# Performance work log

Hardware: AMD Instinct MI355X
Metric: run time of the kernel (lower is better)

Reference implementation:

```python
import jax, jax.numpy as jnp
import numpy as np
from itertools import product

L0 = (41, 1600, 1408)  # sparse_shape (z,y,x) from pc_range / voxel_size + [1,0,0]
B = 4
N_PER = 25000
PNAMES = ['w_in','s_in','b_in','w1','s1','b1','w2a','s2a','b2a','w2b','s2b','b2b','w2c','s2c','b2c','w3a','s3a','b3a','w3b','s3b','b3b','w3c','s3c','b3c','w4a','s4a','b4a','w4b','s4b','b4b','w4c','s4c','b4c','w_out','s_out','b_out']


def _enc(c, shape):
    D, H, W = shape
    return ((c[:, 0].astype(np.int64) * D + c[:, 1]) * H + c[:, 2]) * W + c[:, 3]


def _subm_rb(coords, shape):
    # submanifold conv rulebook: out site i gathers input j with coord_j = coord_i + offset
    N = coords.shape[0]
    keys = _enc(coords, shape)
    order = np.argsort(keys); sk = keys[order]
    ins, outs = [], []
    for dz, dy, dx in product((-1, 0, 1), repeat=3):
        nb = coords.astype(np.int64).copy()
        nb[:, 1] += dz; nb[:, 2] += dy; nb[:, 3] += dx
        ok = ((nb[:, 1] >= 0) & (nb[:, 1] < shape[0]) & (nb[:, 2] >= 0) & (nb[:, 2] < shape[1]) & (nb[:, 3] >= 0) & (nb[:, 3] < shape[2]))
        qi = np.nonzero(ok)[0]
        qk = _enc(nb[qi], shape)
        pos = np.clip(np.searchsorted(sk, qk), 0, N - 1)
        f = sk[pos] == qk
        ins.append(order[pos[f]].astype(np.int32))
        outs.append(qi[f].astype(np.int32))
    R = max(len(a) for a in ins)
    rin = np.zeros((27, R), np.int32); rout = np.full((27, R), N, np.int32)  # pad -> dummy out row
    for k in range(27):
        rin[k, :len(ins[k])] = ins[k]; rout[k, :len(outs[k])] = outs[k]
    return jnp.asarray(rin), jnp.asarray(rout)


def _spconv_rb(coords, shape, ks, st, pd):
    # strided sparse conv: out = (in + pad - k) / stride where divisible and in-bounds
    osh = tuple((shape[i] + 2 * pd[i] - ks[i]) // st[i] + 1 for i in range(3))
    per = []; allk = []
    for off in product(*[range(k) for k in ks]):
        oc = np.empty((coords.shape[0], 4), np.int64)
        oc[:, 0] = coords[:, 0]
        ok = np.ones(coords.shape[0], bool)
        for d in range(3):
            v = coords[:, d + 1].astype(np.int64) + pd[d] - off[d]
            ok &= (v % st[d] == 0)
            v = v // st[d]
            ok &= (v >= 0) & (v < osh[d])
            oc[:, d + 1] = v
        qi = np.nonzero(ok)[0]
        qk = _enc(oc[qi], osh)
        per.append((qi.astype(np.int32), qk)); allk.append(qk)
    uk = np.unique(np.concatenate(allk))
    Nout = len(uk); K = len(per)
    R = max(len(qi) for qi, _ in per)
    rin = np.zeros((K, R), np.int32); rout = np.full((K, R), Nout, np.int32)
    for k, (qi, qk) in enumerate(per):
        rin[k, :len(qi)] = qi
        rout[k, :len(qi)] = np.searchsorted(uk, qk).astype(np.int32)
    t = uk.copy()
    x = t % osh[2]; t //= osh[2]; y = t % osh[1]; t //= osh[1]; z = t % osh[0]; b = t // osh[0]
    ocoords = np.stack([b, z, y, x], 1).astype(np.int32)
    return jnp.asarray(rin), jnp.asarray(rout), ocoords, osh


def _gen_coords(rng):
    # clustered LiDAR-like voxel occupancy: gaussian clusters so 3x3x3 neighborhoods are populated
    out = []
    for b in range(B):
        nc = 250
        ctr = np.stack([rng.integers(6, 34, nc), rng.integers(60, 1540, nc), rng.integers(60, 1348, nc)], 1)
        pts = ctr[np.repeat(np.arange(nc), 400)] + rng.normal(0.0, 2.0, (nc * 400, 3))
        pts = np.rint(pts).astype(np.int64)
        for d in range(3):
            pts[:, d] = np.clip(pts[:, d], 0, L0[d] - 1)
        keys = (pts[:, 0] * L0[1] + pts[:, 1]) * L0[2] + pts[:, 2]
        _, ui = np.unique(keys, return_index=True)
        assert len(ui) >= N_PER
        c = pts[np.sort(ui[:N_PER])]
        out.append(np.concatenate([np.full((N_PER, 1), b, np.int64), c], 1))
    return np.concatenate(out, 0).astype(np.int32)


def _conv(feat, W, rin, rout, nout):
    # gather -> per-offset GEMM -> scatter-add (spconv rulebook algorithm)
    out = jnp.zeros((nout + 1, W.shape[2]), feat.dtype)  # +1 dummy row for padding
    for k in range(W.shape[0]):
        out = out.at[rout[k]].add(feat[rin[k]] @ W[k])
    return out[:nout]


def _bnrelu(x, s, b):
    # eval-mode BatchNorm1d folded to affine, then ReLU
    return jax.nn.relu(x * s + b)


def _net(voxels, normalizer, rb1_in, rb1_out, rb2s_in, rb2s_out, batch2, rb2_in, rb2_out, rb3s_in, rb3s_out, batch3, rb3_in, rb3_out, rb4s_in, rb4s_out, batch4, rb4_in, rb4_out, rbo_in, rbo_out, batch_out, P):
    n0 = voxels.shape[0]; n2 = batch2.shape[0]; n3 = batch3.shape[0]; n4 = batch4.shape[0]; no = batch_out.shape[0]
    f = voxels.sum(1) / normalizer  # mean VFE: (N0, 4)
    x = _bnrelu(_conv(f, P['w_in'], rb1_in, rb1_out, n0), P['s_in'], P['b_in'])
    x = _bnrelu(_conv(x, P['w1'], rb1_in, rb1_out, n0), P['s1'], P['b1'])
    x = _bnrelu(_conv(x, P['w2a'], rb2s_in, rb2s_out, n2), P['s2a'], P['b2a'])
    x = _bnrelu(_conv(x, P['w2b'], rb2_in, rb2_out, n2), P['s2b'], P['b2b'])
    x = _bnrelu(_conv(x, P['w2c'], rb2_in, rb2_out, n2), P['s2c'], P['b2c'])
    x = _bnrelu(_conv(x, P['w3a'], rb3s_in, rb3s_out, n3), P['s3a'], P['b3a'])
    x = _bnrelu(_conv(x, P['w3b'], rb3_in, rb3_out, n3), P['s3b'], P['b3b'])
    x = _bnrelu(_conv(x, P['w3c'], rb3_in, rb3_out, n3), P['s3c'], P['b3c'])
    x = _bnrelu(_conv(x, P['w4a'], rb4s_in, rb4s_out, n4), P['s4a'], P['b4a'])
    x = _bnrelu(_conv(x, P['w4b'], rb4_in, rb4_out, n4), P['s4b'], P['b4b'])
    x = _bnrelu(_conv(x, P['w4c'], rb4_in, rb4_out, n4), P['s4c'], P['b4c'])
    x = _bnrelu(_conv(x, P['w_out'], rbo_in, rbo_out, no), P['s_out'], P['b_out'])
    # per-batch global max pool over active voxels (== F.max_pool1d over voxel dim)
    return jax.ops.segment_max(x, batch_out.astype(jnp.int32), num_segments=B)


def setup_inputs():
    rng = np.random.default_rng(0)
    coords0 = _gen_coords(rng)
    rb1_in, rb1_out = _subm_rb(coords0, L0)
    rb2s_in, rb2s_out, c2, sh2 = _spconv_rb(coords0, L0, (3, 3, 3), (2, 2, 2), (1, 1, 1))
    rb2_in, rb2_out = _subm_rb(c2, sh2)
    rb3s_in, rb3s_out, c3, sh3 = _spconv_rb(c2, sh2, (3, 3, 3), (2, 2, 2), (1, 1, 1))
    rb3_in, rb3_out = _subm_rb(c3, sh3)
    rb4s_in, rb4s_out, c4, sh4 = _spconv_rb(c3, sh3, (3, 3, 3), (2, 2, 2), (0, 1, 1))
    rb4_in, rb4_out = _subm_rb(c4, sh4)
    rbo_in, rbo_out, co, _ = _spconv_rb(c4, sh4, (3, 1, 1), (2, 1, 1), (0, 0, 0))
    N0 = coords0.shape[0]
    d = dict(
        voxels=jnp.asarray(rng.normal(0, 1, (N0, 5, 4)).astype(np.float32)),
        voxel_num_points=jnp.asarray(rng.integers(1, 6, N0).astype(np.int32)),
        voxel_coords=jnp.asarray(coords0),
        rb1_in=rb1_in, rb1_out=rb1_out,
        rb2s_in=rb2s_in, rb2s_out=rb2s_out, batch2=jnp.asarray(c2[:, 0]),
        rb2_in=rb2_in, rb2_out=rb2_out,
        rb3s_in=rb3s_in, rb3s_out=rb3s_out, batch3=jnp.asarray(c3[:, 0]),
        rb3_in=rb3_in, rb3_out=rb3_out,
        rb4s_in=rb4s_in, rb4s_out=rb4s_out, batch4=jnp.asarray(c4[:, 0]),
        rb4_in=rb4_in, rb4_out=rb4_out,
        rbo_in=rbo_in, rbo_out=rbo_out, batch_out=jnp.asarray(co[:, 0]),
    )
    def _w(k, ci, co_):
        return jnp.asarray((rng.normal(0, 1, (k, ci, co_)) / np.sqrt(k * ci)).astype(np.float32))
    def _bn(c):
        return (jnp.asarray(rng.uniform(0.5, 1.5, c).astype(np.float32)), jnp.asarray(rng.normal(0, 0.1, c).astype(np.float32)))
    d['w_in'] = _w(27, 4, 16); d['s_in'], d['b_in'] = _bn(16)
    d['w1'] = _w(27, 16, 16); d['s1'], d['b1'] = _bn(16)
    d['w2a'] = _w(27, 16, 32); d['s2a'], d['b2a'] = _bn(32)
    d['w2b'] = _w(27, 32, 32); d['s2b'], d['b2b'] = _bn(32)
    d['w2c'] = _w(27, 32, 32); d['s2c'], d['b2c'] = _bn(32)
    d['w3a'] = _w(27, 32, 64); d['s3a'], d['b3a'] = _bn(64)
    d['w3b'] = _w(27, 64, 64); d['s3b'], d['b3b'] = _bn(64)
    d['w3c'] = _w(27, 64, 64); d['s3c'], d['b3c'] = _bn(64)
    d['w4a'] = _w(27, 64, 64); d['s4a'], d['b4a'] = _bn(64)
    d['w4b'] = _w(27, 64, 64); d['s4b'], d['b4b'] = _bn(64)
    d['w4c'] = _w(27, 64, 64); d['s4c'], d['b4c'] = _bn(64)
    d['w_out'] = _w(3, 64, 128); d['s_out'], d['b_out'] = _bn(128)
    return d


def reference(voxels, voxel_num_points, voxel_coords, rb1_in, rb1_out, rb2s_in, rb2s_out, batch2, rb2_in, rb2_out, rb3s_in, rb3s_out, batch3, rb3_in, rb3_out, rb4s_in, rb4s_out, batch4, rb4_in, rb4_out, rbo_in, rbo_out, batch_out, w_in, s_in, b_in, w1, s1, b1, w2a, s2a, b2a, w2b, s2b, b2b, w2c, s2c, b2c, w3a, s3a, b3a, w3b, s3b, b3b, w3c, s3c, b3c, w4a, s4a, b4a, w4b, s4b, b4b, w4c, s4c, b4c, w_out, s_out, b_out):
    normalizer = jnp.maximum(voxel_num_points.astype(voxels.dtype), 1.0)[:, None]
    P = dict(zip(PNAMES, (w_in, s_in, b_in, w1, s1, b1, w2a, s2a, b2a, w2b, s2b, b2b, w2c, s2c, b2c, w3a, s3a, b3a, w3b, s3b, b3b, w3c, s3c, b3c, w4a, s4a, b4a, w4b, s4b, b4b, w4c, s4c, b4c, w_out, s_out, b_out)))
    return _net(voxels, normalizer, rb1_in, rb1_out, rb2s_in, rb2s_out, batch2, rb2_in, rb2_out, rb3s_in, rb3s_out, batch3, rb3_in, rb3_out, rb4s_in, rb4s_out, batch4, rb4_in, rb4_out, rbo_in, rbo_out, batch_out, P)
```

## Files before the change

### kernel.cpp

```cpp
#include <hip/hip_runtime.h>
#include <cstddef>
#include <cstdint>

typedef _Float16 half8 __attribute__((ext_vector_type(8)));
typedef float floatx4 __attribute__((ext_vector_type(4)));

static inline int cdiv_i(int a, int b) { return (a + b - 1) / b; }

__global__ void feat_kernel(const float* __restrict__ vox,
                            const int* __restrict__ vnp,
                            _Float16* __restrict__ f, int N0) {
  int t = blockIdx.x * blockDim.x + threadIdx.x;
  if (t >= (N0 + 1) * 8) return;
  int i = t >> 3, c = t & 7;
  float v = 0.f;
  if (i < N0 && c < 4) {
    const float* p = vox + (size_t)i * 20 + c;
    v = (p[0] + p[4] + p[8] + p[12] + p[16]) / fmaxf((float)vnp[i], 1.f);
  }
  f[t] = (_Float16)v;
}

struct RB { const int* rin; const int* rout; int K, R, nout, start, end, off; };
struct RBs { RB d[8]; };
__global__ void rb_fill_all(RBs P, int* __restrict__ tbl, int total) {
  int idx = blockIdx.x * blockDim.x + threadIdx.x;
  if (idx >= total) return;
#pragma unroll
  for (int l = 0; l < 8; ++l) {
    if (idx >= P.d[l].start && idx < P.d[l].end) {
      const RB rb = P.d[l];
      int e = idx - rb.start;
      int o = rb.rout[e];
      if ((unsigned)o < (unsigned)rb.nout) {
        int k = e / rb.R;
        tbl[rb.off + (size_t)k * rb.nout + o] = rb.rin[e];
      }
    }
  }
}

__global__ void tbl_fill_kernel(const int* __restrict__ rin,
                                const int* __restrict__ rout,
                                int* __restrict__ tbl, int K, int R, int nout) {
  int e = blockIdx.x * blockDim.x + threadIdx.x;
  if (e >= K * R) return;
  int o = rout[e];
  if ((unsigned)o >= (unsigned)nout) return;
  int k = e / R;
  tbl[(size_t)k * nout + o] = rin[e];
}

struct WP { const float* W; int K, Ci, CiPad, Co, start, end, off; };
struct WPs { WP d[12]; };
__global__ void wpack_all(WPs P, _Float16* __restrict__ Bp, int total) {
  int idx = blockIdx.x * blockDim.x + threadIdx.x;
  if (idx >= total) return;
#pragma unroll
  for (int l = 0; l < 12; ++l) {
    if (idx >= P.d[l].start && idx < P.d[l].end) {
      const WP w = P.d[l];
      int e = idx - w.start;
      int j = e & 7;
      int lane = (e >> 3) & 63;
      int rest = e >> 9;
      int NT = w.Co >> 4;
      int t = rest % NT, ch = rest / NT;
      int kk = ch * 32 + ((lane >> 4) << 3) + j;
      int k = kk / w.CiPad, ci = kk % w.CiPad;
      int n = t * 16 + (lane & 15);
      float v = (k < w.K && ci < w.Ci)
                    ? w.W[((size_t)k * w.Ci + ci) * w.Co + n]
                    : 0.f;
      Bp[w.off + e] = (_Float16)v;
    }
  }
}

template <int K, int CiPad, int Co, int T, int NTW>
__global__ __launch_bounds__(256) void conv_mfma(
    const _Float16* __restrict__ feat, const _Float16* __restrict__ Bp,
    const int* __restrict__ tbl, const float* __restrict__ sc,
    const float* __restrict__ bi, _Float16* __restrict__ out,
    int nout, int nin) {
  constexpr int NT = Co / 16;
  constexpr int colG = NT / NTW;
  constexpr int rowG = 4 / colG;
  static_assert(4 % colG == 0, "colG must divide 4");
  constexpr int NCH = (K * CiPad + 31) / 32;
  constexpr int L2C = (CiPad == 8) ? 3 : (CiPad == 16) ? 4 : (CiPad == 32) ? 5 : 6;
  if (blockIdx.x == 0 && threadIdx.x < Co)
    out[(size_t)nout * Co + threadIdx.x] = (_Float16)0.f;
  const int wave = threadIdx.x >> 6, lane = threadIdx.x & 63;
  const int rowg = wave / colG, colg = wave % colG;
  const int m = lane & 15;
  const int lb = (lane >> 4) * 8;
  const int i0 = (blockIdx.x * rowG + rowg) * (16 * T);
  if (i0 >= nout) return;

  int rows[T];
#pragma unroll
  for (int t = 0; t < T; ++t) rows[t] = i0 + t * 16 + m;

  int idx[T][NCH];
#pragma unroll
  for (int ch = 0; ch < NCH; ++ch) {
    int ko = (ch * 32 + lb) >> L2C;
#pragma unroll
    for (int t = 0; t < T; ++t) {
      int jj = (rows[t] < nout && ko < K) ? tbl[(size_t)ko * nout + rows[t]] : -1;
      idx[t][ch] = (jj < 0) ? nin : jj;
    }
  }

  floatx4 acc[T][NTW];
#pragma unroll
  for (int t = 0; t < T; ++t)
#pragma unroll
    for (int n = 0; n < NTW; ++n) {
      floatx4 z = {0.f, 0.f, 0.f, 0.f};
      acc[t][n] = z;
    }

  half8 aN[T];
#pragma unroll
  for (int t = 0; t < T; ++t)
    aN[t] = *(const half8*)(feat + (size_t)idx[t][0] * CiPad + (lb & (CiPad - 1)));

#pragma unroll
  for (int ch = 0; ch < NCH; ++ch) {
    half8 aC[T];
#pragma unroll
    for (int t = 0; t < T; ++t) aC[t] = aN[t];
    if (ch + 1 < NCH) {
      int ci0 = ((ch + 1) * 32 + lb) & (CiPad - 1);
#pragma unroll
      for (int t = 0; t < T; ++t)
        aN[t] = *(const half8*)(feat + (size_t)idx[t][ch + 1] * CiPad + ci0);
    }
    const _Float16* bp = Bp + ((size_t)ch * NT * 64 + lane) * 8;
#pragma unroll
    for (int n = 0; n < NTW; ++n) {
      half8 b = *(const half8*)(bp + (colg * NTW + n) * 512);
#pragma unroll
      for (int t = 0; t < T; ++t)
        acc[t][n] =
            __builtin_amdgcn_mfma_f32_16x16x32_f16(aC[t], b, acc[t][n], 0, 0, 0);
    }
  }

#pragma unroll
  for (int n = 0; n < NTW; ++n) {
    int col = (colg * NTW + n) * 16 + m;
    float s_ = sc[col], b_ = bi[col];
#pragma unroll
    for (int t = 0; t < T; ++t) {
#pragma unroll
      for (int r = 0; r < 4; ++r) {
        int orow = i0 + t * 16 + (lane >> 4) * 4 + r;
        if (orow < nout) {
          float v = fmaxf(fmaf(acc[t][n][r], s_, b_), 0.f);
          out[(size_t)orow * Co + col] = (_Float16)v;
        }
      }
    }
  }
}

__global__ __launch_bounds__(256) void segmax2(const _Float16* __restrict__ x,
                                               const int* __restrict__ batch,
                                               int n, float* __restrict__ out) {
  const int RPB = 128;
  int c = threadIdx.x & 127, g = threadIdx.x >> 7;
  int r0 = blockIdx.x * RPB + g;
  int rend = min(n, blockIdx.x * RPB + RPB);
  float mx = 0.f;
  int cb = -1;
  for (int r = r0; r < rend; r += 2) {
    int b = batch[r];
    if (b != cb) {
      if (cb >= 0)
        atomicMax((int*)out + ((size_t)cb << 7) + c, __float_as_int(mx));
      cb = b;
      mx = 0.f;
    }
    mx = fmaxf(mx, (float)x[(size_t)r * 128 + c]);
  }
  if (cb >= 0)
    atomicMax((int*)out + ((size_t)cb << 7) + c, __float_as_int(mx));
}

extern "C" void kernel_launch(void* const* d_in, const int* in_sizes, int n_in,
                              void* d_out, int out_size, void* d_ws, size_t ws_size,
                              hipStream_t stream) {
  auto I = [&](int idx) { return (const int*)d_in[idx]; };
  auto F = [&](int idx) { return (const float*)d_in[idx]; };

  const int N0  = in_sizes[1];
  const int R1  = in_sizes[3] / 27;
  const int R2s = in_sizes[5] / 27;
  const int n2  = in_sizes[7];
  const int R2  = in_sizes[8] / 27;
  const int R3s = in_sizes[10] / 27;
  const int n3  = in_sizes[12];
  const int R3  = in_sizes[13] / 27;
  const int R4s = in_sizes[15] / 27;
  const int n4  = in_sizes[17];
  const int R4  = in_sizes[18] / 27;
  const int Ro  = in_sizes[20] / 3;
  const int no  = in_sizes[22];

  const int wIdx[12] = {23, 26, 29, 32, 35, 38, 41, 44, 47, 50, 53, 56};
  const int Ks[12]   = {27, 27, 27, 27, 27, 27, 27, 27, 27, 27, 27, 3};
  const int Cis[12]  = {4, 16, 16, 32, 32, 32, 64, 64, 64, 64, 64, 64};
  const int Cos[12]  = {16, 16, 32, 32, 32, 64, 64, 64, 64, 64, 64, 128};
  WPs P;
  int wtot = 0;
  int bpOff[12];
  for (int l = 0; l < 12; ++l) {
    int cip = Cis[l] < 8 ? 8 : Cis[l];
    int nch = (Ks[l] * cip + 31) / 32;
    int nt = Cos[l] / 16;
    int sz = nch * nt * 512;
    P.d[l].W = F(wIdx[l]);
    P.d[l].K = Ks[l];  P.d[l].Ci = Cis[l];  P.d[l].CiPad = cip;  P.d[l].Co = Cos[l];
    P.d[l].start = wtot;  P.d[l].end = wtot + sz;  P.d[l].off = wtot;
    bpOff[l] = wtot;
    wtot += sz;
  }

  RBs RP;
  const int rbRin[8]  = {3, 5, 8, 10, 13, 15, 18, 20};
  const int rbRs[8]   = {R1, R2s, R2, R3s, R3, R4s, R4, Ro};
  const int rbKs[8]   = {27, 27, 27, 27, 27, 27, 27, 3};
  const int rbNout[8] = {N0, n2, n2, n3, n3, n4, n4, no};
  size_t tblInts[8];
  size_t tblOff[8];
  size_t totTbl = 0;
  int totFill = 0;
  for (int l = 0; l < 8; ++l) {
    tblInts[l] = (size_t)rbNout[l] * rbKs[l];
    tblOff[l] = totTbl;
    totTbl += tblInts[l];
    RP.d[l].rin = I(rbRin[l]);
    RP.d[l].rout = I(rbRin[l] + 1);
    RP.d[l].K = rbKs[l];  RP.d[l].R = rbRs[l];  RP.d[l].nout = rbNout[l];
    RP.d[l].start = totFill;
    totFill += rbKs[l] * rbRs[l];
    RP.d[l].end = totFill;
    RP.d[l].off = (int)tblOff[l];
  }

  size_t S = (size_t)(N0 + 1) * 16;
  auto smax = [&](size_t v) { if (v > S) S = v; };
  smax((size_t)(n2 + 1) * 32);
  smax((size_t)(n3 + 1) * 64);
  smax((size_t)(n4 + 1) * 64);
  smax((size_t)(no + 1) * 128);
  S = (S + 7) & ~(size_t)7;

  _Float16* h = (_Float16*)d_ws;
  size_t off = 0;
  _Float16* f0 = h + off;   off += (size_t)(N0 + 1) * 8;
  _Float16* bufA = h + off; off += S;
  _Float16* bufB = h + off; off += S;
  _Float16* Bp = h + off;   off += (size_t)((wtot + 7) & ~7);
  int* tblBase = (int*)(h + off);
  size_t usedBytes = off * 2;
  bool prebuilt = (usedBytes + totTbl * 4 <= ws_size);

  feat_kernel<<<cdiv_i((N0 + 1) * 8, 256), 256, 0, stream>>>(F(0), I(1), f0, N0);
  wpack_all<<<cdiv_i(wtot, 256), 256, 0, stream>>>(P, Bp, wtot);
  hipMemsetAsync(d_out, 0, (size_t)out_size * 4, stream);

  const int l2rb[12] = {0, 0, 1, 2, 2, 3, 4, 4, 5, 6, 6, 7};
  const int* tblL[12];
  if (prebuilt) {
    hipMemsetAsync(tblBase, 0xFF, totTbl * 4, stream);
    rb_fill_all<<<cdiv_i(totFill, 256), 256, 0, stream>>>(RP, tblBase, totFill);
    for (int l = 0; l < 12; ++l) tblL[l] = tblBase + tblOff[l2rb[l]];
  } else {
    for (int l = 0; l < 12; ++l) tblL[l] = tblBase;
  }
  auto buildSeq = [&](int rb) {
    if (prebuilt) return;
    hipMemsetAsync(tblBase, 0xFF, tblInts[rb] * 4, stream);
    tbl_fill_kernel<<<cdiv_i(rbKs[rb] * rbRs[rb], 256), 256, 0, stream>>>(
        I(rbRin[rb]), I(rbRin[rb] + 1), tblBase, rbKs[rb], rbRs[rb], rbNout[rb]);
  };

#define CONV(Kk, CIP, CO, Tt, NTWv, IN, LI, OUTB, NOUT, NIN)                  \
  do {                                                                        \
    constexpr int rowsPerBlk = (4 / ((CO / 16) / NTWv)) * 16 * Tt;            \
    conv_mfma<Kk, CIP, CO, Tt, NTWv>                                          \
        <<<cdiv_i(NOUT, rowsPerBlk), 256, 0, stream>>>(                       \
            IN, Bp + bpOff[LI], tblL[LI], F(wIdx[LI] + 1), F(wIdx[LI] + 2),   \
            OUTB, NOUT, NIN);                                                 \
  } while (0)

  buildSeq(0);
  CONV(27, 8, 16, 2, 1, f0, 0, bufA, N0, N0);
  CONV(27, 16, 16, 2, 1, bufA, 1, bufB, N0, N0);
  buildSeq(1);
  CONV(27, 16, 32, 2, 2, bufB, 2, bufA, n2, N0);
  buildSeq(2);
  CONV(27, 32, 32, 2, 2, bufA, 3, bufB, n2, n2);
  CONV(27, 32, 32, 2, 2, bufB, 4, bufA, n2, n2);
  buildSeq(3);
  CONV(27, 32, 64, 2, 2, bufA, 5, bufB, n3, n2);
  buildSeq(4);
  CONV(27, 64, 64, 1, 2, bufB, 6, bufA, n3, n3);
  CONV(27, 64, 64, 1, 2, bufA, 7, bufB, n3, n3);
  buildSeq(5);
  CONV(27, 64, 64, 1, 2, bufB, 8, bufA, n4, n3);
  buildSeq(6);
  CONV(27, 64, 64, 1, 2, bufA, 9, bufB, n4, n4);
  CONV(27, 64, 64, 1, 2, bufB, 10, bufA, n4, n4);
  buildSeq(7);
  CONV(3, 64, 128, 1, 4, bufA, 11, bufB, no, n4);

  segmax2<<<cdiv_i(no, 128), 256, 0, stream>>>(bufB, I(22), no, (float*)d_out);
#undef CONV
}
```

Baseline: 483.3 us.

## Split kernel-offset reduction across waves with LDS reduce and deeper load prefetch

Reworks the sparse-conv MFMA kernel so waves in a block can split the 27 kernel offsets (split-K) and combine partial sums through shared memory, with each wave handling one 16-row tile. It also adds multi-stage register prefetch of gathered features and weight fragments (4-deep for A, 2-deep for B). Per-layer configs are retuned so the deep, low-row-count layers use more split-K parallelism. The aim is more parallelism and better latency hiding on small layers, at the cost of LDS traffic, a block barrier, and less row reuse of the loaded weight tiles.

```diff
diff --git a/kernel.cpp b/kernel.cpp
--- a/kernel.cpp
+++ b/kernel.cpp
@@ -77,92 +77,176 @@
   }
 }
 
-template <int K, int CiPad, int Co, int T, int NTW>
+template <int K, int CiPad, int Co, int KS, int CG>
 __global__ __launch_bounds__(256) void conv_mfma(
     const _Float16* __restrict__ feat, const _Float16* __restrict__ Bp,
     const int* __restrict__ tbl, const float* __restrict__ sc,
     const float* __restrict__ bi, _Float16* __restrict__ out,
     int nout, int nin) {
   constexpr int NT = Co / 16;
-  constexpr int colG = NT / NTW;
-  constexpr int rowG = 4 / colG;
-  static_assert(4 % colG == 0, "colG must divide 4");
+  constexpr int NTW = NT / CG;
+  constexpr int RG = 4 / (KS * CG);
+  static_assert(KS * CG * RG == 4 && RG >= 1 && NT % CG == 0);
+  constexpr int DIV = (CiPad >= 32) ? (CiPad / 32) : 1;
   constexpr int NCH = (K * CiPad + 31) / 32;
-  constexpr int L2C = (CiPad == 8) ? 3 : (CiPad == 16) ? 4 : (CiPad == 32) ? 5 : 6;
+  constexpr int L2C = (CiPad == 8) ? 3 : 4;
+  constexpr int CoP = Co + 4;
+
+  __shared__ float red[(KS > 1) ? (KS - 1) * RG * 16 * CoP : 1];
+
   if (blockIdx.x == 0 && threadIdx.x < Co)
     out[(size_t)nout * Co + threadIdx.x] = (_Float16)0.f;
+
   const int wave = threadIdx.x >> 6, lane = threadIdx.x & 63;
-  const int rowg = wave / colG, colg = wave % colG;
-  const int m = lane & 15;
-  const int lb = (lane >> 4) * 8;
-  const int i0 = (blockIdx.x * rowG + rowg) * (16 * T);
-  if (i0 >= nout) return;
-
-  int rows[T];
-#pragma unroll
-  for (int t = 0; t < T; ++t) rows[t] = i0 + t * 16 + m;
-
-  int idx[T][NCH];
-#pragma unroll
-  for (int ch = 0; ch < NCH; ++ch) {
-    int ko = (ch * 32 + lb) >> L2C;
-#pragma unroll
-    for (int t = 0; t < T; ++t) {
-      int jj = (rows[t] < nout && ko < K) ? tbl[(size_t)ko * nout + rows[t]] : -1;
-      idx[t][ch] = (jj < 0) ? nin : jj;
-    }
-  }
-
-  floatx4 acc[T][NTW];
-#pragma unroll
-  for (int t = 0; t < T; ++t)
-#pragma unroll
-    for (int n = 0; n < NTW; ++n) {
-      floatx4 z = {0.f, 0.f, 0.f, 0.f};
-      acc[t][n] = z;
-    }
-
-  half8 aN[T];
-#pragma unroll
-  for (int t = 0; t < T; ++t)
-    aN[t] = *(const half8*)(feat + (size_t)idx[t][0] * CiPad + (lb & (CiPad - 1)));
-
-#pragma unroll
-  for (int ch = 0; ch < NCH; ++ch) {
-    half8 aC[T];
-#pragma unroll
-    for (int t = 0; t < T; ++t) aC[t] = aN[t];
-    if (ch + 1 < NCH) {
-      int ci0 = ((ch + 1) * 32 + lb) & (CiPad - 1);
-#pragma unroll
-      for (int t = 0; t < T; ++t)
-        aN[t] = *(const half8*)(feat + (size_t)idx[t][ch + 1] * CiPad + ci0);
-    }
-    const _Float16* bp = Bp + ((size_t)ch * NT * 64 + lane) * 8;
-#pragma unroll
-    for (int n = 0; n < NTW; ++n) {
-      half8 b = *(const half8*)(bp + (colg * NTW + n) * 512);
-#pragma unroll
-      for (int t = 0; t < T; ++t)
-        acc[t][n] =
-            __builtin_amdgcn_mfma_f32_16x16x32_f16(aC[t], b, acc[t][n], 0, 0, 0);
-    }
-  }
-
+  const int ks = wave % KS;
+  const int cg = (wave / KS) % CG;
+  const int rowg = wave / (KS * CG);
+  const int m = lane & 15, lb = (lane >> 4) * 8;
+  const int i0 = (blockIdx.x * RG + rowg) * 16;
+  if constexpr (KS == 1) {
+    if (i0 >= nout) return;
+  }
+  const int row = i0 + m;
+  const bool rOK = row < nout;
+
+  floatx4 acc[NTW];
 #pragma unroll
   for (int n = 0; n < NTW; ++n) {
-    int col = (colg * NTW + n) * 16 + m;
+    floatx4 z = {0.f, 0.f, 0.f, 0.f};
+    acc[n] = z;
+  }
+
+  if constexpr (CiPad >= 32) {
+    constexpr int NKW = (K + KS - 1) / KS;
+    constexpr int NC = NKW * DIV;
+    constexpr int DA = NC < 4 ? NC : 4;
+    constexpr int DB = NC < 2 ? NC : 2;
+    int idx[NKW];
+#pragma unroll
+    for (int q = 0; q < NKW; ++q) {
+      int k = ks + q * KS;
+      int jj = (rOK && k < K) ? tbl[(size_t)k * nout + row] : -1;
+      idx[q] = (jj < 0) ? nin : jj;
+    }
+    half8 ap[DA];
+    half8 bq[DB][NTW];
+#pragma unroll
+    for (int d = 0; d < DA; ++d)
+      ap[d] = *(const half8*)(feat + (size_t)idx[d / DIV] * CiPad +
+                              (d % DIV) * 32 + lb);
+#pragma unroll
+    for (int d = 0; d < DB; ++d) {
+      int k = ks + (d / DIV) * KS;
+      int ch = ((k < K) ? k : (K - 1)) * DIV + (d % DIV);
+#pragma unroll
+      for (int n = 0; n < NTW; ++n)
+        bq[d][n] = *(const half8*)(Bp + ((size_t)ch * NT * 64 + lane) * 8 +
+                                   (size_t)(cg * NTW + n) * 512);
+    }
+#pragma unroll
+    for (int ii = 0; ii < NC; ++ii) {
+      half8 a = ap[ii % DA];
+      half8 bt[NTW];
+#pragma unroll
+      for (int n = 0; n < NTW; ++n) bt[n] = bq[ii % DB][n];
+      if (ii + DA < NC) {
+        int nx = ii + DA;
+        ap[ii % DA] = *(const half8*)(feat + (size_t)idx[nx / DIV] * CiPad +
+                                      (nx % DIV) * 32 + lb);
+      }
+      if (ii + DB < NC) {
+        int nx = ii + DB;
+        int k = ks + (nx / DIV) * KS;
+        int ch = ((k < K) ? k : (K - 1)) * DIV + (nx % DIV);
+#pragma unroll
+        for (int n = 0; n < NTW; ++n)
+          bq[ii % DB][n] = *(const half8*)(Bp + ((size_t)ch * NT * 64 + lane) * 8 +
+                                           (size_t)(cg * NTW + n) * 512);
+      }
+#pragma unroll
+      for (int n = 0; n < NTW; ++n)
+        acc[n] = __builtin_amdgcn_mfma_f32_16x16x32_f16(a, bt[n], acc[n], 0, 0, 0);
+    }
+  } else {
+    constexpr int NC = NCH;
+    constexpr int DA = NC < 4 ? NC : 4;
+    constexpr int DB = NC < 2 ? NC : 2;
+    int idx[NC];
+#pragma unroll
+    for (int q = 0; q < NC; ++q) {
+      int ko = (q * 32 + lb) >> L2C;
+      int jj = (rOK && ko < K) ? tbl[(size_t)ko * nout + row] : -1;
+      idx[q] = (jj < 0) ? nin : jj;
+    }
+    half8 ap[DA];
+    half8 bq[DB][NTW];
+#pragma unroll
+    for (int d = 0; d < DA; ++d)
+      ap[d] = *(const half8*)(feat + (size_t)idx[d] * CiPad +
+                              ((d * 32 + lb) & (CiPad - 1)));
+#pragma unroll
+    for (int d = 0; d < DB; ++d)
+#pragma unroll
+      for (int n = 0; n < NTW; ++n)
+        bq[d][n] = *(const half8*)(Bp + ((size_t)d * NT * 64 + lane) * 8 +
+                                   (size_t)(cg * NTW + n) * 512);
+#pragma unroll
+    for (int ii = 0; ii < NC; ++ii) {
+      half8 a = ap[ii % DA];
+      half8 bt[NTW];
+#pragma unroll
+      for (int n = 0; n < NTW; ++n) bt[n] = bq[ii % DB][n];
+      if (ii + DA < NC) {
+        int nx = ii + DA;
+        ap[ii % DA] = *(const half8*)(feat + (size_t)idx[nx] * CiPad +
+                                      ((nx * 32 + lb) & (CiPad - 1)));
+      }
+      if (ii + DB < NC) {
+        int nx = ii + DB;
+#pragma unroll
+        for (int n = 0; n < NTW; ++n)
+          bq[ii % DB][n] = *(const half8*)(Bp + ((size_t)nx * NT * 64 + lane) * 8 +
+                                           (size_t)(cg * NTW + n) * 512);
+      }
+#pragma unroll
+      for (int n = 0; n < NTW; ++n)
+        acc[n] = __builtin_amdgcn_mfma_f32_16x16x32_f16(a, bt[n], acc[n], 0, 0, 0);
+    }
+  }
+
+  const int rl = (lane >> 4) * 4;
+  if constexpr (KS > 1) {
+    if (ks > 0) {
+#pragma unroll
+      for (int n = 0; n < NTW; ++n) {
+        int col = (cg * NTW + n) * 16 + m;
+#pragma unroll
+        for (int r = 0; r < 4; ++r)
+          red[((ks - 1) * RG + rowg) * 16 * CoP + (rl + r) * CoP + col] = acc[n][r];
+      }
+    }
+    __syncthreads();
+    if (ks > 0) return;
+#pragma unroll
+    for (int s = 1; s < KS; ++s)
+#pragma unroll
+      for (int n = 0; n < NTW; ++n) {
+        int col = (cg * NTW + n) * 16 + m;
+#pragma unroll
+        for (int r = 0; r < 4; ++r)
+          acc[n][r] += red[((s - 1) * RG + rowg) * 16 * CoP + (rl + r) * CoP + col];
+      }
+  }
+
+#pragma unroll
+  for (int n = 0; n < NTW; ++n) {
+    int col = (cg * NTW + n) * 16 + m;
     float s_ = sc[col], b_ = bi[col];
 #pragma unroll
-    for (int t = 0; t < T; ++t) {
-#pragma unroll
-      for (int r = 0; r < 4; ++r) {
-        int orow = i0 + t * 16 + (lane >> 4) * 4 + r;
-        if (orow < nout) {
-          float v = fmaxf(fmaf(acc[t][n][r], s_, b_), 0.f);
-          out[(size_t)orow * Co + col] = (_Float16)v;
-        }
-      }
+    for (int r = 0; r < 4; ++r) {
+      int orow = i0 + rl + r;
+      if (orow < nout)
+        out[(size_t)orow * Co + col] = (_Float16)fmaxf(fmaf(acc[n][r], s_, b_), 0.f);
     }
   }
 }
@@ -289,36 +373,35 @@
         I(rbRin[rb]), I(rbRin[rb] + 1), tblBase, rbKs[rb], rbRs[rb], rbNout[rb]);
   };
 
-#define CONV(Kk, CIP, CO, Tt, NTWv, IN, LI, OUTB, NOUT, NIN)                  \
+#define CONV(Kk, CIP, CO, KSv, CGv, IN, LI, OUTB, NOUT, NIN)                  \
   do {                                                                        \
-    constexpr int rowsPerBlk = (4 / ((CO / 16) / NTWv)) * 16 * Tt;            \
-    conv_mfma<Kk, CIP, CO, Tt, NTWv>                                          \
+    constexpr int rowsPerBlk = (4 / (KSv * CGv)) * 16;                        \
+    conv_mfma<Kk, CIP, CO, KSv, CGv>                                          \
         <<<cdiv_i(NOUT, rowsPerBlk), 256, 0, stream>>>(                       \
             IN, Bp + bpOff[LI], tblL[LI], F(wIdx[LI] + 1), F(wIdx[LI] + 2),   \
             OUTB, NOUT, NIN);                                                 \
   } while (0)
 
   buildSeq(0);
-  CONV(27, 8, 16, 2, 1, f0, 0, bufA, N0, N0);
-  CONV(27, 16, 16, 2, 1, bufA, 1, bufB, N0, N0);
+  CONV(27, 8, 16, 1, 1, f0, 0, bufA, N0, N0);
+  CONV(27, 16, 16, 1, 1, bufA, 1, bufB, N0, N0);
   buildSeq(1);
-  CONV(27, 16, 32, 2, 2, bufB, 2, bufA, n2, N0);
+  CONV(27, 16, 32, 1, 1, bufB, 2, bufA, n2, N0);
   buildSeq(2);
-  CONV(27, 32, 32, 2, 2, bufA, 3, bufB, n2, n2);
-  CONV(27, 32, 32, 2, 2, bufB, 4, bufA, n2, n2);
+  CONV(27, 32, 32, 1, 1, bufA, 3, bufB, n2, n2);
+  CONV(27, 32, 32, 1, 1, bufB, 4, bufA, n2, n2);
   buildSeq(3);
-  CONV(27, 32, 64, 2, 2, bufA, 5, bufB, n3, n2);
+  CONV(27, 32, 64, 2, 1, bufA, 5, bufB, n3, n2);
   buildSeq(4);
-  CONV(27, 64, 64, 1, 2, bufB, 6, bufA, n3, n3);
-  CONV(27, 64, 64, 1, 2, bufA, 7, bufB, n3, n3);
+  CONV(27, 64, 64, 2, 1, bufB, 6, bufA, n3, n3);
+  CONV(27, 64, 64, 2, 1, bufA, 7, bufB, n3, n3);
   buildSeq(5);
-  CONV(27, 64, 64, 1, 2, bufB, 8, bufA, n4, n3);
+  CONV(27, 64, 64, 4, 1, bufB, 8, bufA, n4, n3);
   buildSeq(6);
-  CONV(27, 64, 64, 1, 2, bufA, 9, bufB, n4, n4);
-  CONV(27, 64, 64, 1, 2, bufB, 10, bufA, n4, n4);
+  CONV(27, 64, 64, 4, 1, bufA, 9, bufB, n4, n4);
+  CONV(27, 64, 64, 4, 1, bufB, 10, bufA, n4, n4);
   buildSeq(7);
-  CONV(3, 64, 128, 1, 4, bufA, 11, bufB, no, n4);
-
+  CONV(3, 64, 128, 2, 2, bufA, 11, bufB, no, n4);
   segmax2<<<cdiv_i(no, 128), 256, 0, stream>>>(bufB, I(22), no, (float*)d_out);
 #undef CONV
 }
```

Measured after the change: 464.0 us. 1.04x faster.
